# Kernel tuning notes

Measured on AMD Instinct MI355X. Metric: run time of the kernel, lower is better.

The kernel has to match this reference:

```python
import jax, jax.numpy as jnp
import numpy as np

DIM = 1024
B, S = 2, 2048

def _gelu(v):
    return jax.nn.gelu(v, approximate=False)

def setup_inputs() -> dict:
    key = jax.random.key(0)
    ks = jax.random.split(key, 24)
    d = DIM
    def lin(k, fan_in, fan_out):
        k1, k2 = jax.random.split(k)
        bound = 1.0 / np.sqrt(fan_in)
        W = jax.random.uniform(k1, (fan_in, fan_out), jnp.float32, -bound, bound)
        b = jax.random.uniform(k2, (fan_out,), jnp.float32, -bound, bound)
        return W, b
    w_pt1, b_pt1 = lin(ks[0], d, 2 * d)
    w_pt2, b_pt2 = lin(ks[1], 2 * d, d)
    w_wg, b_wg = lin(ks[2], d, d)
    w_mag, b_mag = lin(ks[3], d, d)
    w_q1, b_q1 = lin(ks[4], d, d)
    w_q2, b_q2 = lin(ks[5], d, d)
    w_mix, b_mix = lin(ks[6], d, 2 * d)
    w_o1, b_o1 = lin(ks[7], d, d)
    w_o2, b_o2 = lin(ks[8], d, d)
    return {
        "x": jax.random.normal(ks[9], (B, S, d), jnp.float32),
        "w_pt1": w_pt1, "b_pt1": b_pt1, "w_pt2": w_pt2, "b_pt2": b_pt2,
        "int_scale": jnp.ones((d,), jnp.float32) * 0.001,
        "w_wg": w_wg, "b_wg": b_wg,
        "gate_temp": jnp.ones((1,), jnp.float32) * 2.0,
        "w_mag": w_mag, "b_mag": b_mag,
        "w_q1": w_q1, "b_q1": b_q1, "w_q2": w_q2, "b_q2": b_q2,
        "w_mix": w_mix, "b_mix": b_mix,
        "ln_g": jnp.ones((d,), jnp.float32), "ln_b": jnp.zeros((d,), jnp.float32),
        "w_o1": w_o1, "b_o1": b_o1, "w_o2": w_o2, "b_o2": b_o2,
    }

def reference(x, w_pt1, b_pt1, w_pt2, b_pt2, int_scale, w_wg, b_wg, gate_temp,
              w_mag, b_mag, w_q1, b_q1, w_q2, b_q2, w_mix, b_mix,
              ln_g, ln_b, w_o1, b_o1, w_o2, b_o2):
    # input-dependent phase basis
    phase_delta = _gelu(x @ w_pt1 + b_pt1) @ w_pt2 + b_pt2          # [B,S,D]
    phi = jnp.cumsum(phase_delta * jnp.abs(int_scale), axis=1)
    # selective write gate + magnitude
    write_gate = jax.nn.sigmoid((x @ w_wg + b_wg) * gate_temp)
    magnitude = jax.nn.sigmoid(x @ w_mag + b_mag) * 5.0
    content = write_gate * x * magnitude
    # complex-phase memory accumulation (4 seq-length scans)
    memory_real = jnp.cumsum(content * jnp.cos(phi), axis=1)
    memory_imag = jnp.cumsum(content * jnp.sin(phi), axis=1)
    accum_weight = jnp.cumsum(write_gate * magnitude + 1e-8, axis=1)
    inv_s = 1.0 / jnp.sqrt(accum_weight)
    mr, mi = memory_real * inv_s, memory_imag * inv_s
    # query-phase retrieval (complex rotation)
    query_phase = phi + (_gelu(x @ w_q1 + b_q1) @ w_q2 + b_q2)
    cq, sq = jnp.cos(query_phase), jnp.sin(query_phase)
    retrieved_real = mr * cq + mi * sq
    retrieved_imag = mi * cq - mr * sq
    # input-dependent output mixing
    mix = x @ w_mix + b_mix
    d = x.shape[-1]
    mix_real = jax.nn.sigmoid(mix[..., :d])
    mix_imag = jax.nn.sigmoid(mix[..., d:])
    retrieved = mix_real * retrieved_real + mix_imag * retrieved_imag
    # output head: LayerNorm -> Linear -> GELU -> (Dropout=identity in eval) -> Linear
    mu = jnp.mean(retrieved, axis=-1, keepdims=True)
    var = jnp.var(retrieved, axis=-1, keepdims=True)
    ln = (retrieved - mu) / jnp.sqrt(var + 1e-5) * ln_g + ln_b
    out = _gelu(ln @ w_o1 + b_o1) @ w_o2 + b_o2
    return x + out
```

## Files before the change

kernel.cpp:

```cpp
#include <hip/hip_runtime.h>
#include <hip/hip_bf16.h>

#define MTOT 4096
#define DD   1024
#define D2   2048
#define SS   2048
#define BB   2
#define NC2  64
#define CL2  (SS/NC2)

typedef __attribute__((ext_vector_type(8))) short bf16x8;
typedef __attribute__((ext_vector_type(4))) float f32x4;

__device__ __forceinline__ float sigmf(float v){
    return 1.0f/(1.0f+__expf(-v));
}
__device__ __forceinline__ float geluf(float v){
    float u = 0.7978845608f*v*(1.0f + 0.044715f*v*v);
    float e = __expf(2.0f*u);
    float t = 1.0f - 2.0f/(e + 1.0f);
    return 0.5f*v*(1.0f + t);
}
__device__ __forceinline__ ushort f2bf(float f){
    unsigned u = __float_as_uint(f);
    unsigned r = (u + 0x7FFF + ((u>>16)&1)) >> 16;
    return (ushort)r;
}
__device__ __forceinline__ float bf2f(ushort u){
    return __uint_as_float(((unsigned)u)<<16);
}

__device__ __forceinline__ void stage_tile(
    const ushort* __restrict__ A, const ushort* __restrict__ Bt, int K,
    int m0, int n0, int k0, ushort* As, ushort* Bs)
{
    int tid = threadIdx.x;
    #pragma unroll
    for (int i = 0; i < 2; i++) {
        int e = (i*256 + tid) * 8;
        int r = e >> 5, c = e & 31;
        __builtin_amdgcn_global_load_lds(
            (const __attribute__((address_space(1))) void*)(A + (size_t)(m0 + r)*K + k0 + c),
            (__attribute__((address_space(3))) void*)(As + e), 16, 0, 0);
        __builtin_amdgcn_global_load_lds(
            (const __attribute__((address_space(1))) void*)(Bt + (size_t)(n0 + r)*K + k0 + c),
            (__attribute__((address_space(3))) void*)(Bs + e), 16, 0, 0);
    }
}

__device__ __forceinline__ void compute_step(
    const ushort* As, const ushort* Bs, int wr, int wc, int lrow, int lk8,
    f32x4 (&acc)[4][4])
{
    bf16x8 af[4], bfr[4];
    #pragma unroll
    for (int i = 0; i < 4; i++) {
        af[i]  = *(const bf16x8*)(As + (wr*64 + i*16 + lrow)*32 + lk8);
        bfr[i] = *(const bf16x8*)(Bs + (wc*64 + i*16 + lrow)*32 + lk8);
    }
    #pragma unroll
    for (int i = 0; i < 4; i++)
        #pragma unroll
        for (int j = 0; j < 4; j++)
            acc[i][j] = __builtin_amdgcn_mfma_f32_16x16x32_bf16(af[i], bfr[j], acc[i][j], 0, 0, 0);
}

__device__ __forceinline__ void mgemm_core(
    const ushort* __restrict__ A, const ushort* __restrict__ Bt, int K,
    int m0, int n0, ushort (&As)[2][4096], ushort (&Bs)[2][4096], f32x4 (&acc)[4][4])
{
    int lane = threadIdx.x & 63, wave = threadIdx.x >> 6;
    int wr = wave >> 1, wc = wave & 1;
    int lrow = lane & 15, lk8 = (lane >> 4) << 3;
    stage_tile(A, Bt, K, m0, n0, 0, As[0], Bs[0]);
    __syncthreads();
    int NT = K >> 5;
    int cur = 0;
    for (int t = 0; t < NT-1; t++) {
        stage_tile(A, Bt, K, m0, n0, (t+1) << 5, As[cur^1], Bs[cur^1]);
        compute_step(As[cur], Bs[cur], wr, wc, lrow, lk8, acc);
        __syncthreads();
        cur ^= 1;
    }
    compute_step(As[cur], Bs[cur], wr, wc, lrow, lk8, acc);
}

__global__ __launch_bounds__(256,4) void mgemmA_k(
    const ushort* __restrict__ xb, const ushort* __restrict__ Wt,
    const float* __restrict__ b_pt1, const float* __restrict__ b_wg,
    const float* __restrict__ b_mag, const float* __restrict__ b_q1,
    const float* __restrict__ b_mix, const float* __restrict__ gtemp,
    ushort* __restrict__ H1b, ushort* __restrict__ wgb, ushort* __restrict__ magb,
    ushort* __restrict__ Hqb, ushort* __restrict__ mixb)
{
    __shared__ ushort As[2][4096], Bs[2][4096];
    int bid = blockIdx.x;
    int xcd = bid & 7, local = bid >> 3;
    int m0 = (xcd*4 + (local & 3)) * 128;
    int n0 = (local >> 2) * 128;
    f32x4 acc[4][4] = {};
    mgemm_core(xb, Wt, 1024, m0, n0, As, Bs, acc);
    int lane = threadIdx.x & 63, wave = threadIdx.x >> 6;
    int wr = wave >> 1, wc = wave & 1;
    int rng = n0 >> 10;
    float gt = gtemp[0];
    #pragma unroll
    for (int i = 0; i < 4; i++) {
        int mb = m0 + wr*64 + i*16 + (lane>>4)*4;
        #pragma unroll
        for (int j = 0; j < 4; j++) {
            int n = n0 + wc*64 + j*16 + (lane&15);
            #pragma unroll
            for (int r = 0; r < 4; r++) {
                int m = mb + r;
                float v = acc[i][j][r];
                if (rng < 2) {
                    H1b[(size_t)m*D2 + n] = f2bf(geluf(v + b_pt1[n]));
                } else if (rng == 2) {
                    wgb[(size_t)m*DD + n-2048] = f2bf(sigmf((v + b_wg[n-2048])*gt));
                } else if (rng == 3) {
                    magb[(size_t)m*DD + n-3072] = f2bf(sigmf(v + b_mag[n-3072])*5.0f);
                } else if (rng == 4) {
                    Hqb[(size_t)m*DD + n-4096] = f2bf(geluf(v + b_q1[n-4096]));
                } else {
                    mixb[(size_t)m*D2 + n-5120] = f2bf(sigmf(v + b_mix[n-5120]));
                }
            }
        }
    }
}

__global__ __launch_bounds__(256,4) void mgemmBC_k(
    const ushort* __restrict__ H1b, const ushort* __restrict__ wt_pt2,
    const ushort* __restrict__ Hqb, const ushort* __restrict__ wt_q2,
    const float* __restrict__ b_pt2, const float* __restrict__ b_q2,
    const float* __restrict__ iscale,
    float* __restrict__ pd, float* __restrict__ qadj)
{
    __shared__ ushort As[2][4096], Bs[2][4096];
    int bid = blockIdx.x;
    int xcd = bid & 7, local = bid >> 3;
    int m0 = (xcd*4 + (local & 3)) * 128;
    int rest = local >> 2;
    int z = rest >> 3;
    int n0 = (rest & 7) * 128;
    const ushort* A  = z ? Hqb   : H1b;
    const ushort* Bt = z ? wt_q2 : wt_pt2;
    const float* bias = z ? b_q2 : b_pt2;
    int K = z ? 1024 : 2048;
    float* outp = z ? qadj : pd;
    f32x4 acc[4][4] = {};
    mgemm_core(A, Bt, K, m0, n0, As, Bs, acc);
    int lane = threadIdx.x & 63, wave = threadIdx.x >> 6;
    int wr = wave >> 1, wc = wave & 1;
    #pragma unroll
    for (int i = 0; i < 4; i++) {
        int mb = m0 + wr*64 + i*16 + (lane>>4)*4;
        #pragma unroll
        for (int j = 0; j < 4; j++) {
            int n = n0 + wc*64 + j*16 + (lane&15);
            float bv = bias[n];
            float sc = z ? 1.0f : fabsf(iscale[n]);
            #pragma unroll
            for (int r = 0; r < 4; r++) {
                float v = acc[i][j][r] + bv;
                outp[(size_t)(mb+r)*DD + n] = z ? v : v*sc;
            }
        }
    }
}

template<int ACT, bool RESID, bool OUTBF16>
__global__ __launch_bounds__(256,4) void mgemm_k(
    const ushort* __restrict__ A, const ushort* __restrict__ Bt,
    const float* __restrict__ bias, const float* __restrict__ resid,
    void* __restrict__ Cout, int N, int K)
{
    __shared__ ushort As[2][4096], Bs[2][4096];
    int bid = blockIdx.x;
    int xcd = bid & 7, local = bid >> 3;
    int m0 = (xcd*4 + (local & 3)) * 128;
    int n0 = (local >> 2) * 128;
    f32x4 acc[4][4] = {};
    mgemm_core(A, Bt, K, m0, n0, As, Bs, acc);
    int lane = threadIdx.x & 63, wave = threadIdx.x >> 6;
    int wr = wave >> 1, wc = wave & 1;
    #pragma unroll
    for (int i = 0; i < 4; i++) {
        int mb = m0 + wr*64 + i*16 + (lane>>4)*4;
        #pragma unroll
        for (int j = 0; j < 4; j++) {
            int n = n0 + wc*64 + j*16 + (lane&15);
            float bv = bias[n];
            #pragma unroll
            for (int r = 0; r < 4; r++) {
                size_t idx = (size_t)(mb + r)*N + n;
                float v = acc[i][j][r] + bv;
                if (ACT==1) v = geluf(v);
                if (RESID) v += resid[idx];
                if (OUTBF16) ((ushort*)Cout)[idx] = f2bf(v);
                else         ((float*)Cout)[idx]  = v;
            }
        }
    }
}

__global__ __launch_bounds__(256) void cvt_bf16_k(const float* __restrict__ in, ushort* __restrict__ outp){
    size_t i = ((size_t)blockIdx.x*256 + threadIdx.x)*8;
    float4 a = *(const float4*)(in + i);
    float4 b = *(const float4*)(in + i + 4);
    ushort t[8];
    t[0]=f2bf(a.x); t[1]=f2bf(a.y); t[2]=f2bf(a.z); t[3]=f2bf(a.w);
    t[4]=f2bf(b.x); t[5]=f2bf(b.y); t[6]=f2bf(b.z); t[7]=f2bf(b.w);
    *(int4*)(outp + i) = *(const int4*)t;
}

__device__ __forceinline__ void tcvt_body(const float* W, ushort* Wt, int K, int N){
    __shared__ float tile[32][33];
    int n0 = blockIdx.x*32, k0 = blockIdx.y*32;
    int tx = threadIdx.x & 7, ty = threadIdx.x >> 3;
    float4 v = *(const float4*)(W + (size_t)(k0+ty)*N + n0 + tx*4);
    tile[ty][tx*4+0]=v.x; tile[ty][tx*4+1]=v.y; tile[ty][tx*4+2]=v.z; tile[ty][tx*4+3]=v.w;
    __syncthreads();
    ushort t[4];
    #pragma unroll
    for (int i=0;i<4;i++) t[i] = f2bf(tile[tx*4+i][ty]);
    *(uint2*)(Wt + (size_t)(n0+ty)*K + k0 + tx*4) = *(const uint2*)t;
}

__global__ __launch_bounds__(256) void tcvt_k(const float* __restrict__ W, ushort* __restrict__ Wt, int K, int N){
    tcvt_body(W, Wt, K, N);
}
__global__ __launch_bounds__(256) void tcvt2_k(const float* __restrict__ w0, ushort* __restrict__ o0,
                                               const float* __restrict__ w1, ushort* __restrict__ o1){
    tcvt_body(blockIdx.z ? w1 : w0, blockIdx.z ? o1 : o0, 1024, 2048);
}
__global__ __launch_bounds__(256) void tcvt6_k(
    const float* __restrict__ w0, ushort* __restrict__ o0,
    const float* __restrict__ w1, ushort* __restrict__ o1,
    const float* __restrict__ w2, ushort* __restrict__ o2,
    const float* __restrict__ w3, ushort* __restrict__ o3,
    const float* __restrict__ w4, ushort* __restrict__ o4,
    const float* __restrict__ w5, ushort* __restrict__ o5)
{
    const float* W; ushort* Wt;
    switch(blockIdx.z){
        case 0: W=w0; Wt=o0; break;
        case 1: W=w1; Wt=o1; break;
        case 2: W=w2; Wt=o2; break;
        case 3: W=w3; Wt=o3; break;
        case 4: W=w4; Wt=o4; break;
        default: W=w5; Wt=o5; break;
    }
    tcvt_body(W, Wt, 1024, 1024);
}

__global__ __launch_bounds__(256) void passA_k(
    const float* __restrict__ pd, float* __restrict__ csum)
{
    int d = blockIdx.x*256 + threadIdx.x;
    int c = blockIdx.y, b = blockIdx.z;
    const float* p = pd + ((size_t)b*SS + (size_t)c*CL2)*DD + d;
    float s = 0.f;
    for (int i = 0; i < CL2; i++) s += p[(size_t)i*DD];
    csum[((size_t)b*NC2 + c)*DD + d] = s;
}

__global__ void scan2_k(float* __restrict__ csum, int nchains){
    int idx = blockIdx.x*256 + threadIdx.x;
    if (idx >= nchains) return;
    int xg = idx / DD, d = idx % DD;
    float* p = csum + (size_t)xg*NC2*DD + d;
    float run = 0.f;
    for (int c = 0; c < NC2; c++){ float t = p[(size_t)c*DD]; p[(size_t)c*DD] = run; run += t; }
}

__global__ __launch_bounds__(256) void passB_k(
    const float* __restrict__ pd, const ushort* __restrict__ wgb,
    const ushort* __restrict__ magb, const float* __restrict__ x,
    const float* __restrict__ csum_phi, float* __restrict__ csum_tri)
{
    int d = blockIdx.x*256 + threadIdx.x;
    int c = blockIdx.y, b = blockIdx.z;
    size_t off = ((size_t)b*SS + (size_t)c*CL2)*DD + d;
    float ph = csum_phi[((size_t)b*NC2 + c)*DD + d];
    float s0=0.f, s1=0.f, s2=0.f;
    for (int i = 0; i < CL2; i++){
        size_t o = off + (size_t)i*DD;
        ph += pd[o];
        float w = bf2f(wgb[o]), m = bf2f(magb[o]);
        float ct = w*x[o]*m;
        float sp, cp; sincosf(ph, &sp, &cp);
        s0 += ct*cp; s1 += ct*sp; s2 += fmaf(w, m, 1e-8f);
    }
    size_t cs = ((size_t)b*NC2 + c)*DD + d;
    size_t G = (size_t)BB*NC2*DD;
    csum_tri[cs]=s0; csum_tri[G+cs]=s1; csum_tri[2*G+cs]=s2;
}

__global__ __launch_bounds__(256) void passC_k(
    const float* __restrict__ pd, const ushort* __restrict__ wgb,
    const ushort* __restrict__ magb, const float* __restrict__ x,
    const float* __restrict__ qadj, const ushort* __restrict__ mixb,
    const float* __restrict__ csum_phi, const float* __restrict__ csum_tri,
    ushort* __restrict__ ret)
{
    int d = blockIdx.x*256 + threadIdx.x;
    int c = blockIdx.y, b = blockIdx.z;
    size_t off = ((size_t)b*SS + (size_t)c*CL2)*DD + d;
    size_t cs = ((size_t)b*NC2 + c)*DD + d;
    size_t G = (size_t)BB*NC2*DD;
    float ph = csum_phi[cs];
    float r0 = csum_tri[cs], r1 = csum_tri[G+cs], r2 = csum_tri[2*G+cs];
    size_t row0 = (size_t)b*SS + (size_t)c*CL2;
    for (int i = 0; i < CL2; i++){
        size_t o = off + (size_t)i*DD;
        ph += pd[o];
        float w = bf2f(wgb[o]), m = bf2f(magb[o]);
        float ct = w*x[o]*m;
        float sp, cp; sincosf(ph, &sp, &cp);
        r0 += ct*cp; r1 += ct*sp; r2 += fmaf(w, m, 1e-8f);
        float inv = rsqrtf(r2);
        float mr = r0*inv, mi = r1*inv;
        float q = ph + qadj[o];
        float sq, cq; sincosf(q, &sq, &cq);
        float rr = mr*cq + mi*sq;
        float ri = mi*cq - mr*sq;
        size_t mb2 = (row0 + i)*D2 + d;
        ret[o] = f2bf(bf2f(mixb[mb2])*rr + bf2f(mixb[mb2+DD])*ri);
    }
}

__global__ __launch_bounds__(256) void ln_k(
    const ushort* __restrict__ ret, const float* __restrict__ ln_g,
    const float* __restrict__ ln_b, ushort* __restrict__ outp)
{
    int row = blockIdx.x;
    size_t base = (size_t)row*DD;
    float vals[4];
    float sum=0.f, sumsq=0.f;
    #pragma unroll
    for (int k = 0; k < 4; k++){
        int d = threadIdx.x + k*256;
        float v = bf2f(ret[base+d]);
        vals[k]=v; sum+=v; sumsq = fmaf(v,v,sumsq);
    }
    #pragma unroll
    for (int off=32; off; off>>=1){
        sum   += __shfl_down(sum,off);
        sumsq += __shfl_down(sumsq,off);
    }
    __shared__ float red[8];
    int lane = threadIdx.x & 63, wid = threadIdx.x >> 6;
    if (lane==0){ red[wid]=sum; red[4+wid]=sumsq; }
    __syncthreads();
    sum   = red[0]+red[1]+red[2]+red[3];
    sumsq = red[4]+red[5]+red[6]+red[7];
    float mu  = sum * (1.0f/DD);
    float var = sumsq*(1.0f/DD) - mu*mu;
    float rstd = rsqrtf(var + 1e-5f);
    #pragma unroll
    for (int k = 0; k < 4; k++){
        int d = threadIdx.x + k*256;
        outp[base+d] = f2bf((vals[k]-mu)*rstd*ln_g[d] + ln_b[d]);
    }
}

extern "C" void kernel_launch(void* const* d_in, const int* in_sizes, int n_in,
                              void* d_out, int out_size, void* d_ws, size_t ws_size,
                              hipStream_t stream)
{
    const float* x     = (const float*)d_in[0];
    const float* w_pt1 = (const float*)d_in[1];
    const float* b_pt1 = (const float*)d_in[2];
    const float* w_pt2 = (const float*)d_in[3];
    const float* b_pt2 = (const float*)d_in[4];
    const float* iscale= (const float*)d_in[5];
    const float* w_wg  = (const float*)d_in[6];
    const float* b_wg  = (const float*)d_in[7];
    const float* gtemp = (const float*)d_in[8];
    const float* w_mag = (const float*)d_in[9];
    const float* b_mag = (const float*)d_in[10];
    const float* w_q1  = (const float*)d_in[11];
    const float* b_q1  = (const float*)d_in[12];
    const float* w_q2  = (const float*)d_in[13];
    const float* b_q2  = (const float*)d_in[14];
    const float* w_mix = (const float*)d_in[15];
    const float* b_mix = (const float*)d_in[16];
    const float* ln_g  = (const float*)d_in[17];
    const float* ln_b  = (const float*)d_in[18];
    const float* w_o1  = (const float*)d_in[19];
    const float* b_o1  = (const float*)d_in[20];
    const float* w_o2  = (const float*)d_in[21];
    const float* b_o2  = (const float*)d_in[22];
    float* out = (float*)d_out;

    const size_t SZ = (size_t)MTOT*DD;
    ushort* u = (ushort*)d_ws;
    ushort* xb    = u;                 u += SZ;
    ushort* H1b   = u;                 u += 2*SZ;
    ushort* ret   = H1b;
    ushort* Hqb   = u;                 u += SZ;
    ushort* lnb   = Hqb;
    ushort* wgb   = u;                 u += SZ;
    ushort* magb  = u;                 u += SZ;
    ushort* mixb  = u;                 u += 2*SZ;
    ushort* Hob   = u;                 u += SZ;
    float*  pd    = (float*)u;         u += 2*SZ;
    float*  qadj  = (float*)u;         u += 2*SZ;
    ushort* Wt_all= u;                 u += (size_t)7168*1024;
    ushort* wt_pt2= u;                 u += (size_t)1024*2048;
    ushort* wt_q2 = u;                 u += (size_t)1024*1024;
    ushort* wt_o1 = u;                 u += (size_t)1024*1024;
    ushort* wt_o2 = u;                 u += (size_t)1024*1024;
    float* csum_phi = (float*)u;
    float* csum_tri = csum_phi + (size_t)BB*NC2*DD;

    dim3 blk(256);
    cvt_bf16_k<<<dim3(SZ/2048), blk, 0, stream>>>(x, xb);
    tcvt2_k<<<dim3(64, 32, 2), blk, 0, stream>>>(w_pt1, Wt_all, w_mix, Wt_all + (size_t)5120*1024);
    tcvt6_k<<<dim3(32, 32, 6), blk, 0, stream>>>(
        w_wg,  Wt_all + (size_t)2048*1024,
        w_mag, Wt_all + (size_t)3072*1024,
        w_q1,  Wt_all + (size_t)4096*1024,
        w_q2,  wt_q2,  w_o1, wt_o1,  w_o2, wt_o2);
    tcvt_k<<<dim3(32, 64), blk, 0, stream>>>(w_pt2, wt_pt2, 2048, 1024);
    mgemmA_k<<<dim3(1792), blk, 0, stream>>>(xb, Wt_all, b_pt1, b_wg, b_mag, b_q1, b_mix,
                                             gtemp, H1b, wgb, magb, Hqb, mixb);
    mgemmBC_k<<<dim3(512), blk, 0, stream>>>(H1b, wt_pt2, Hqb, wt_q2, b_pt2, b_q2,
                                             iscale, pd, qadj);
    passA_k<<<dim3(DD/256, NC2, BB), blk, 0, stream>>>(pd, csum_phi);
    scan2_k<<<dim3((BB*DD+255)/256), blk, 0, stream>>>(csum_phi, BB*DD);
    passB_k<<<dim3(DD/256, NC2, BB), blk, 0, stream>>>(pd, wgb, magb, x, csum_phi, csum_tri);
    scan2_k<<<dim3((3*BB*DD+255)/256), blk, 0, stream>>>(csum_tri, 3*BB*DD);
    passC_k<<<dim3(DD/256, NC2, BB), blk, 0, stream>>>(pd, wgb, magb, x, qadj, mixb,
                                                       csum_phi, csum_tri, ret);
    ln_k<<<dim3(MTOT), blk, 0, stream>>>(ret, ln_g, ln_b, lnb);
    mgemm_k<1,false,true><<<dim3(256), blk, 0, stream>>>(lnb, wt_o1, b_o1, nullptr, Hob, DD, DD);
    mgemm_k<0,true,false><<<dim3(256), blk, 0, stream>>>(Hob, wt_o2, b_o2, x, out, DD, DD);
}
```

Measured before the change: 281.4 us.

## Swizzle GEMM LDS tiles, deepen prefetch pipeline, read bf16 x in scans

The shared GEMM core now XOR-swizzles the 16-byte chunks of each LDS row to avoid bank conflicts on fragment reads. It also issues two tiles ahead, using explicit vmcnt/lgkmcnt waits and raw barriers, so fragments are pulled into registers before the buffer is refilled. MFMA blocks are wrapped in setprio to favour the math waves. Separately, the scan passes read the bf16 copy of x instead of fp32, halving that traffic at some cost in precision for the content term.

```diff
diff --git a/kernel.cpp b/kernel.cpp
--- a/kernel.cpp
+++ b/kernel.cpp
@@ -38,7 +38,9 @@
     #pragma unroll
     for (int i = 0; i < 2; i++) {
         int e = (i*256 + tid) * 8;
-        int r = e >> 5, c = e & 31;
+        int r = e >> 5;
+        int s = (e >> 3) & 3;
+        int c = ((s ^ ((r >> 1) & 3)) << 3);
         __builtin_amdgcn_global_load_lds(
             (const __attribute__((address_space(1))) void*)(A + (size_t)(m0 + r)*K + k0 + c),
             (__attribute__((address_space(3))) void*)(As + e), 16, 0, 0);
@@ -48,21 +50,29 @@
     }
 }
 
-__device__ __forceinline__ void compute_step(
-    const ushort* As, const ushort* Bs, int wr, int wc, int lrow, int lk8,
-    f32x4 (&acc)[4][4])
-{
-    bf16x8 af[4], bfr[4];
+__device__ __forceinline__ void load_frags(
+    const ushort* As, const ushort* Bs, int wr, int wc, int lrow, int cs,
+    bf16x8 (&af)[4], bf16x8 (&bfr)[4])
+{
     #pragma unroll
     for (int i = 0; i < 4; i++) {
-        af[i]  = *(const bf16x8*)(As + (wr*64 + i*16 + lrow)*32 + lk8);
-        bfr[i] = *(const bf16x8*)(Bs + (wc*64 + i*16 + lrow)*32 + lk8);
-    }
+        int ra = wr*64 + i*16 + lrow;
+        int rb = wc*64 + i*16 + lrow;
+        af[i]  = *(const bf16x8*)(As + ra*32 + ((cs ^ ((ra>>1)&3))<<3));
+        bfr[i] = *(const bf16x8*)(Bs + rb*32 + ((cs ^ ((rb>>1)&3))<<3));
+    }
+}
+
+__device__ __forceinline__ void do_mfma(
+    const bf16x8 (&af)[4], const bf16x8 (&bfr)[4], f32x4 (&acc)[4][4])
+{
+    __builtin_amdgcn_s_setprio(1);
     #pragma unroll
     for (int i = 0; i < 4; i++)
         #pragma unroll
         for (int j = 0; j < 4; j++)
             acc[i][j] = __builtin_amdgcn_mfma_f32_16x16x32_bf16(af[i], bfr[j], acc[i][j], 0, 0, 0);
+    __builtin_amdgcn_s_setprio(0);
 }
 
 __device__ __forceinline__ void mgemm_core(
@@ -71,18 +81,28 @@
 {
     int lane = threadIdx.x & 63, wave = threadIdx.x >> 6;
     int wr = wave >> 1, wc = wave & 1;
-    int lrow = lane & 15, lk8 = (lane >> 4) << 3;
-    stage_tile(A, Bt, K, m0, n0, 0, As[0], Bs[0]);
-    __syncthreads();
+    int lrow = lane & 15, cs = lane >> 4;
     int NT = K >> 5;
-    int cur = 0;
-    for (int t = 0; t < NT-1; t++) {
-        stage_tile(A, Bt, K, m0, n0, (t+1) << 5, As[cur^1], Bs[cur^1]);
-        compute_step(As[cur], Bs[cur], wr, wc, lrow, lk8, acc);
-        __syncthreads();
-        cur ^= 1;
-    }
-    compute_step(As[cur], Bs[cur], wr, wc, lrow, lk8, acc);
+    stage_tile(A, Bt, K, m0, n0, 0,  As[0], Bs[0]);
+    stage_tile(A, Bt, K, m0, n0, 32, As[1], Bs[1]);
+    for (int t = 0; t < NT-1; ++t) {
+        asm volatile("s_waitcnt vmcnt(4)" ::: "memory");
+        __builtin_amdgcn_s_barrier();
+        bf16x8 af[4], bfr[4];
+        load_frags(As[t&1], Bs[t&1], wr, wc, lrow, cs, af, bfr);
+        if (t < NT-2) {
+            asm volatile("s_waitcnt lgkmcnt(0)" ::: "memory");
+            __builtin_amdgcn_s_barrier();
+            stage_tile(A, Bt, K, m0, n0, (t+2) << 5, As[t&1], Bs[t&1]);
+        }
+        __builtin_amdgcn_sched_barrier(0);
+        do_mfma(af, bfr, acc);
+    }
+    asm volatile("s_waitcnt vmcnt(0)" ::: "memory");
+    __builtin_amdgcn_s_barrier();
+    bf16x8 af[4], bfr[4];
+    load_frags(As[(NT-1)&1], Bs[(NT-1)&1], wr, wc, lrow, cs, af, bfr);
+    do_mfma(af, bfr, acc);
 }
 
 __global__ __launch_bounds__(256,4) void mgemmA_k(
@@ -277,7 +297,7 @@
 
 __global__ __launch_bounds__(256) void passB_k(
     const float* __restrict__ pd, const ushort* __restrict__ wgb,
-    const ushort* __restrict__ magb, const float* __restrict__ x,
+    const ushort* __restrict__ magb, const ushort* __restrict__ xb,
     const float* __restrict__ csum_phi, float* __restrict__ csum_tri)
 {
     int d = blockIdx.x*256 + threadIdx.x;
@@ -289,7 +309,7 @@
         size_t o = off + (size_t)i*DD;
         ph += pd[o];
         float w = bf2f(wgb[o]), m = bf2f(magb[o]);
-        float ct = w*x[o]*m;
+        float ct = w*bf2f(xb[o])*m;
         float sp, cp; sincosf(ph, &sp, &cp);
         s0 += ct*cp; s1 += ct*sp; s2 += fmaf(w, m, 1e-8f);
     }
@@ -300,7 +320,7 @@
 
 __global__ __launch_bounds__(256) void passC_k(
     const float* __restrict__ pd, const ushort* __restrict__ wgb,
-    const ushort* __restrict__ magb, const float* __restrict__ x,
+    const ushort* __restrict__ magb, const ushort* __restrict__ xb,
     const float* __restrict__ qadj, const ushort* __restrict__ mixb,
     const float* __restrict__ csum_phi, const float* __restrict__ csum_tri,
     ushort* __restrict__ ret)
@@ -317,7 +337,7 @@
         size_t o = off + (size_t)i*DD;
         ph += pd[o];
         float w = bf2f(wgb[o]), m = bf2f(magb[o]);
-        float ct = w*x[o]*m;
+        float ct = w*bf2f(xb[o])*m;
         float sp, cp; sincosf(ph, &sp, &cp);
         r0 += ct*cp; r1 += ct*sp; r2 += fmaf(w, m, 1e-8f);
         float inv = rsqrtf(r2);
@@ -431,9 +451,9 @@
                                              iscale, pd, qadj);
     passA_k<<<dim3(DD/256, NC2, BB), blk, 0, stream>>>(pd, csum_phi);
     scan2_k<<<dim3((BB*DD+255)/256), blk, 0, stream>>>(csum_phi, BB*DD);
-    passB_k<<<dim3(DD/256, NC2, BB), blk, 0, stream>>>(pd, wgb, magb, x, csum_phi, csum_tri);
+    passB_k<<<dim3(DD/256, NC2, BB), blk, 0, stream>>>(pd, wgb, magb, xb, csum_phi, csum_tri);
     scan2_k<<<dim3((3*BB*DD+255)/256), blk, 0, stream>>>(csum_tri, 3*BB*DD);
-    passC_k<<<dim3(DD/256, NC2, BB), blk, 0, stream>>>(pd, wgb, magb, x, qadj, mixb,
+    passC_k<<<dim3(DD/256, NC2, BB), blk, 0, stream>>>(pd, wgb, magb, xb, qadj, mixb,
                                                        csum_phi, csum_tri, ret);
     ln_k<<<dim3(MTOT), blk, 0, stream>>>(ret, ln_g, ln_b, lnb);
     mgemm_k<1,false,true><<<dim3(256), blk, 0, stream>>>(lnb, wt_o1, b_o1, nullptr, Hob, DD, DD);
```

Result: faster. 267.2 us (-5.0%).
